# Optimization experiments

Measured on AMD Instinct MI355X. Metric: run time of the kernel, lower is better.

Reference implementation:

```python
import jax, jax.numpy as jnp
import numpy as np

N, D, H, E = 50000, 128, 512, 500000

def setup_inputs() -> dict:
    key = jax.random.key(0)
    k1, k2, k3, k4 = jax.random.split(key, 4)
    z = jax.random.normal(k1, (N, D), dtype=jnp.float32)
    edge_index = jax.random.randint(k2, (2, E), 0, N, dtype=jnp.int64)
    # torch Linear weights: fc1 [H, 2D], fc2 [1, H]
    W1 = jax.random.normal(k3, (H, 2 * D), dtype=jnp.float32) * (1.0 / np.sqrt(2 * D))
    b1 = jnp.zeros((H,), dtype=jnp.float32)
    W2 = jax.random.normal(k4, (1, H), dtype=jnp.float32) * (1.0 / np.sqrt(H))
    b2 = jnp.zeros((1,), dtype=jnp.float32)
    return {"z": z, "edge_index": edge_index, "W1": W1, "b1": b1, "W2": W2, "b2": b2}

def reference(z, edge_index, W1, b1, W2, b2):
    # gather endpoints and concat along feature dim: [E, 2D]
    z_cat = jnp.concatenate([z[edge_index[0]], z[edge_index[1]]], axis=1)
    # dropout is identity at eval (drop_rate effectively 0 for the baseline)
    h = jax.nn.relu(jnp.einsum('ef,hf->eh', z_cat, W1) + b1)  # [E, H]
    y = (jnp.einsum('eh,oh->eo', h, W2) + b2).reshape(-1)     # [E]
    return y
```

## Files before the change

kernel.cpp:

```cpp
#include <hip/hip_runtime.h>


typedef __bf16 bf16x8 __attribute__((ext_vector_type(8)));
typedef float f32x4 __attribute__((ext_vector_type(4)));

__device__ __forceinline__ unsigned short f2b(float f) {
    unsigned int u = __float_as_uint(f);
    u = (u + 0x7fffu + ((u >> 16) & 1u)) >> 16;
    return (unsigned short)u;
}

__device__ __forceinline__ void gload_lds16(const unsigned short* g, unsigned short* l) {
    __builtin_amdgcn_global_load_lds(
        (const __attribute__((address_space(1))) unsigned int*)g,
        (__attribute__((address_space(3))) unsigned int*)l, 16, 0, 0);
}

__global__ void prep_kernel(const float* __restrict__ z, const float* __restrict__ W1,
                            unsigned short* __restrict__ zb, unsigned short* __restrict__ w1s,
                            int nz4) {
    int stride = gridDim.x * blockDim.x;
    const int nw = 256 * 64;
    const int total = nz4 + nw;
    for (int idx = blockIdx.x * blockDim.x + threadIdx.x; idx < total; idx += stride) {
        if (idx < nz4) {
            float4 v = ((const float4*)z)[idx];
            ushort4 o;
            o.x = f2b(v.x); o.y = f2b(v.y); o.z = f2b(v.z); o.w = f2b(v.w);
            ((ushort4*)zb)[idx] = o;
        } else {
            int u = idx - nz4;
            int lane = u & 63;
            int blk  = u >> 6;
            int h  = (blk >> 3) * 16 + (lane & 15);
            int kb = (blk & 7) * 32 + (lane >> 4) * 8;
            const float* src = W1 + h * 256 + kb;
            ushort4 o0, o1;
            float4 v0 = *(const float4*)(src);
            float4 v1 = *(const float4*)(src + 4);
            o0.x = f2b(v0.x); o0.y = f2b(v0.y); o0.z = f2b(v0.z); o0.w = f2b(v0.w);
            o1.x = f2b(v1.x); o1.y = f2b(v1.y); o1.z = f2b(v1.z); o1.w = f2b(v1.w);
            ushort4* dst = (ushort4*)(w1s + u * 8);
            dst[0] = o0; dst[1] = o1;
        }
    }
}

__global__ __launch_bounds__(512, 2)
void edge_mlp_kernel(const int* __restrict__ ei, const unsigned short* __restrict__ zb,
                     const unsigned short* __restrict__ w1s,
                     const float* __restrict__ b1, const float* __restrict__ W2,
                     const float* __restrict__ b2p, float* __restrict__ out,
                     int E, int ntiles) {
    __shared__ unsigned short ldsA[2][64 * 256];
    __shared__ float ldsY[512];
    __shared__ float ldsB1[512];

    const int tid  = threadIdx.x;
    const int lane = tid & 63;
    const int w    = tid >> 6;
    const int l15  = lane & 15;
    const int l4   = lane >> 4;
    const int G    = gridDim.x;

    const int t0 = blockIdx.x;
    if (t0 >= ntiles) return;

    ldsB1[tid] = b1[tid];

    uint4 breg[4][8];
    #pragma unroll
    for (int j = 0; j < 4; ++j)
        #pragma unroll
        for (int kc = 0; kc < 8; ++kc)
            breg[j][kc] = *(const uint4*)(w1s + (((w * 4 + j) * 8 + kc) << 9) + lane * 8);

    f32x4 w2v[4];
    #pragma unroll
    for (int j = 0; j < 4; ++j)
        w2v[j] = *(const f32x4*)&W2[w * 64 + j * 16 + l4 * 4];
    const float b2v = b2p[0];

    const int side = (lane >> 4) & 1;
    const int rsub = lane >> 5;
    const int swz  = l15 & 7;

    asm volatile("s_waitcnt vmcnt(0)" ::: "memory");

    int ival[4];
    #pragma unroll
    for (int it = 0; it < 4; ++it) {
        int e = t0 * 64 + w * 8 + it * 2 + rsub;
        e = (e < E) ? e : (E - 1);
        ival[it] = ei[side * E + e];
    }
    #pragma unroll
    for (int it = 0; it < 4; ++it) {
        int s15 = l15 ^ ((it * 2 + rsub) & 7);
        gload_lds16(zb + (ival[it] << 7) + (s15 << 3),
                    &ldsA[0][(w * 8 + it * 2) << 8]);
    }
    asm volatile("" ::: "memory");
    {
        int t1 = t0 + G;
        #pragma unroll
        for (int it = 0; it < 4; ++it) {
            int e = t1 * 64 + w * 8 + it * 2 + rsub;
            e = (e < E) ? e : (E - 1);
            ival[it] = ei[side * E + e];
        }
    }

    int cur = 0;
    for (int t = t0; t < ntiles; t += G) {
        asm volatile("s_waitcnt vmcnt(4)" ::: "memory");
        __builtin_amdgcn_s_barrier();
        asm volatile("" ::: "memory");

        const unsigned short* bufc = &ldsA[cur][0];
        unsigned short* bufn = &ldsA[cur ^ 1][0];

        f32x4 acc[4][4];
        {
            f32x4 b1t[4];
            #pragma unroll
            for (int j = 0; j < 4; ++j)
                b1t[j] = *(const f32x4*)&ldsB1[w * 64 + j * 16 + l4 * 4];
            #pragma unroll
            for (int i = 0; i < 4; i++)
                #pragma unroll
                for (int j = 0; j < 4; j++) acc[i][j] = b1t[j];
        }

        __builtin_amdgcn_s_setprio(1);
        #pragma unroll
        for (int kc = 0; kc < 4; ++kc) {
            bf16x8 a[4];
            #pragma unroll
            for (int i = 0; i < 4; ++i)
                a[i] = *(const bf16x8*)&bufc[((l15 + 16 * i) << 8) + ((((kc << 2) + l4) ^ swz) << 3)];
            #pragma unroll
            for (int i = 0; i < 4; ++i)
                #pragma unroll
                for (int j = 0; j < 4; ++j)
                    acc[i][j] = __builtin_amdgcn_mfma_f32_16x16x32_bf16(
                        *(const bf16x8*)&breg[j][kc], a[i], acc[i][j], 0, 0, 0);
        }
        __builtin_amdgcn_s_setprio(0);

        #pragma unroll
        for (int it = 0; it < 4; ++it) {
            int s15 = l15 ^ ((it * 2 + rsub) & 7);
            gload_lds16(zb + (ival[it] << 7) + (s15 << 3),
                        bufn + ((w * 8 + it * 2) << 8));
        }
        asm volatile("" ::: "memory");

        __builtin_amdgcn_s_setprio(1);
        #pragma unroll
        for (int kc = 4; kc < 8; ++kc) {
            bf16x8 a[4];
            #pragma unroll
            for (int i = 0; i < 4; ++i)
                a[i] = *(const bf16x8*)&bufc[((l15 + 16 * i) << 8) + ((((kc << 2) + l4) ^ swz) << 3)];
            #pragma unroll
            for (int i = 0; i < 4; ++i)
                #pragma unroll
                for (int j = 0; j < 4; ++j)
                    acc[i][j] = __builtin_amdgcn_mfma_f32_16x16x32_bf16(
                        *(const bf16x8*)&breg[j][kc], a[i], acc[i][j], 0, 0, 0);
        }
        __builtin_amdgcn_s_setprio(0);

        {
            int tt = t + 2 * G;
            #pragma unroll
            for (int it = 0; it < 4; ++it) {
                int e = tt * 64 + w * 8 + it * 2 + rsub;
                e = (e < E) ? e : (E - 1);
                ival[it] = ei[side * E + e];
            }
        }

        #pragma unroll
        for (int i = 0; i < 4; i++) {
            float s = 0.f;
            #pragma unroll
            for (int j = 0; j < 4; j++)
                #pragma unroll
                for (int r = 0; r < 4; r++)
                    s = fmaf(fmaxf(acc[i][j][r], 0.f), w2v[j][r], s);
            s += __shfl_xor(s, 16);
            s += __shfl_xor(s, 32);
            if (l4 == 0) ldsY[w * 64 + i * 16 + l15] = s;
        }
        asm volatile("s_waitcnt lgkmcnt(0)" ::: "memory");
        __builtin_amdgcn_s_barrier();
        asm volatile("" ::: "memory");
        if (tid < 64) {
            int e = t * 64 + tid;
            if (e < E) {
                float v = b2v;
                #pragma unroll
                for (int k = 0; k < 8; ++k) v += ldsY[k * 64 + tid];
                out[e] = v;
            }
        }

        cur ^= 1;
    }
}

extern "C" void kernel_launch(void* const* d_in, const int* in_sizes, int n_in,
                              void* d_out, int out_size, void* d_ws, size_t ws_size,
                              hipStream_t stream) {
    const float* z  = (const float*)d_in[0];
    const int*   ei = (const int*)d_in[1];
    const float* W1 = (const float*)d_in[2];
    const float* b1 = (const float*)d_in[3];
    const float* W2 = (const float*)d_in[4];
    const float* b2 = (const float*)d_in[5];
    float* out = (float*)d_out;

    const int E  = in_sizes[1] / 2;
    const int NZ = in_sizes[0];

    unsigned short* zb  = (unsigned short*)d_ws;
    unsigned short* w1s = zb + NZ;

    prep_kernel<<<2048, 256, 0, stream>>>(z, W1, zb, w1s, NZ / 4);

    const int ntiles = (E + 63) / 64;
    int grid = ntiles < 512 ? ntiles : 512;
    edge_mlp_kernel<<<grid, 512, 0, stream>>>(ei, zb, w1s, b1, W2, b2, out, E, ntiles);
}
```

Before: 212.8 us.

## Triple-buffer gathered rows, preload edge indices into LDS, defer output reduction

Each block now preloads the edge indices for all of its tiles into LDS once at the start, instead of loading indices from global memory every iteration. The z-row gathers use three LDS buffers with a prefetch distance of two tiles, and the K loop is no longer split around the gather issue. The per-tile output reduction is deferred to the next iteration using a double-buffered ldsY and spread across all waves, which removes one barrier per tile. The index preload assumes at most 16 tiles per block, which holds for this grid and edge count. The extra buffer and index array use more LDS per block.

```diff
diff --git a/kernel.cpp b/kernel.cpp
--- a/kernel.cpp
+++ b/kernel.cpp
@@ -52,8 +52,9 @@
                      const float* __restrict__ b1, const float* __restrict__ W2,
                      const float* __restrict__ b2p, float* __restrict__ out,
                      int E, int ntiles) {
-    __shared__ unsigned short ldsA[2][64 * 256];
-    __shared__ float ldsY[512];
+    __shared__ unsigned short ldsA[3][64 * 256];
+    __shared__ int   ldsIdx[16 * 128];
+    __shared__ float ldsY[2][512];
     __shared__ float ldsB1[512];
 
     const int tid  = threadIdx.x;
@@ -62,10 +63,22 @@
     const int l15  = lane & 15;
     const int l4   = lane >> 4;
     const int G    = gridDim.x;
-
-    const int t0 = blockIdx.x;
+    const int t0   = blockIdx.x;
     if (t0 >= ntiles) return;
 
+    {
+        const int itq = tid >> 7;
+        const int sd  = (tid >> 6) & 1;
+        const int m   = tid & 63;
+        #pragma unroll
+        for (int p = 0; p < 4; ++p) {
+            int itt = p * 4 + itq;
+            int t = t0 + itt * G;
+            int e = t * 64 + m;
+            if (t >= ntiles || e >= E) e = E - 1;
+            ldsIdx[itt * 128 + sd * 64 + m] = ei[sd * E + e];
+        }
+    }
     ldsB1[tid] = b1[tid];
 
     uint4 breg[4][8];
@@ -83,42 +96,51 @@
 
     const int side = (lane >> 4) & 1;
     const int rsub = lane >> 5;
-    const int swz  = l15 & 7;
-
-    asm volatile("s_waitcnt vmcnt(0)" ::: "memory");
-
-    int ival[4];
-    #pragma unroll
-    for (int it = 0; it < 4; ++it) {
-        int e = t0 * 64 + w * 8 + it * 2 + rsub;
-        e = (e < E) ? e : (E - 1);
-        ival[it] = ei[side * E + e];
-    }
-    #pragma unroll
-    for (int it = 0; it < 4; ++it) {
-        int s15 = l15 ^ ((it * 2 + rsub) & 7);
-        gload_lds16(zb + (ival[it] << 7) + (s15 << 3),
-                    &ldsA[0][(w * 8 + it * 2) << 8]);
-    }
+
+    asm volatile("s_waitcnt vmcnt(0) lgkmcnt(0)" ::: "memory");
+    __builtin_amdgcn_s_barrier();
     asm volatile("" ::: "memory");
-    {
-        int t1 = t0 + G;
-        #pragma unroll
-        for (int it = 0; it < 4; ++it) {
-            int e = t1 * 64 + w * 8 + it * 2 + rsub;
-            e = (e < E) ? e : (E - 1);
-            ival[it] = ei[side * E + e];
-        }
-    }
-
-    int cur = 0;
-    for (int t = t0; t < ntiles; t += G) {
+
+#define ISSUE_GATHER(ITIDX, BUF)                                              \
+    do {                                                                      \
+        _Pragma("unroll")                                                     \
+        for (int q_ = 0; q_ < 4; ++q_) {                                      \
+            int m_   = w * 8 + q_ * 2 + rsub;                                 \
+            int row_ = ldsIdx[(ITIDX) * 128 + side * 64 + m_];                \
+            int s15_ = l15 ^ (m_ & 7);                                        \
+            gload_lds16(zb + (row_ << 7) + (s15_ << 3),                       \
+                        &ldsA[BUF][(w * 8 + q_ * 2) << 8]);                   \
+        }                                                                     \
+    } while (0)
+
+    ISSUE_GATHER(0, 0);
+    ISSUE_GATHER(1, 1);
+
+    int tprev = 0, pprev = 0, it = 0;
+    for (int t = t0; t < ntiles; t += G, ++it) {
+        const int p = it & 1;
         asm volatile("s_waitcnt vmcnt(4)" ::: "memory");
+        asm volatile("s_waitcnt lgkmcnt(0)" ::: "memory");
         __builtin_amdgcn_s_barrier();
         asm volatile("" ::: "memory");
 
-        const unsigned short* bufc = &ldsA[cur][0];
-        unsigned short* bufn = &ldsA[cur ^ 1][0];
+        if (it > 0 && lane < 8) {
+            int e = tprev * 64 + w * 8 + lane;
+            if (e < E) {
+                float v = b2v;
+                #pragma unroll
+                for (int k = 0; k < 8; ++k) v += ldsY[pprev][k * 64 + w * 8 + lane];
+                out[e] = v;
+            }
+        }
+
+        {
+            int itg = it + 2; if (itg > 15) itg = 15;
+            ISSUE_GATHER(itg, (it + 2) % 3);
+        }
+        asm volatile("" ::: "memory");
+
+        const unsigned short* bufc = &ldsA[it % 3][0];
 
         f32x4 acc[4][4];
         {
@@ -132,9 +154,10 @@
                 for (int j = 0; j < 4; j++) acc[i][j] = b1t[j];
         }
 
+        const int swz = l15 & 7;
         __builtin_amdgcn_s_setprio(1);
         #pragma unroll
-        for (int kc = 0; kc < 4; ++kc) {
+        for (int kc = 0; kc < 8; ++kc) {
             bf16x8 a[4];
             #pragma unroll
             for (int i = 0; i < 4; ++i)
@@ -147,40 +170,6 @@
                         *(const bf16x8*)&breg[j][kc], a[i], acc[i][j], 0, 0, 0);
         }
         __builtin_amdgcn_s_setprio(0);
-
-        #pragma unroll
-        for (int it = 0; it < 4; ++it) {
-            int s15 = l15 ^ ((it * 2 + rsub) & 7);
-            gload_lds16(zb + (ival[it] << 7) + (s15 << 3),
-                        bufn + ((w * 8 + it * 2) << 8));
-        }
-        asm volatile("" ::: "memory");
-
-        __builtin_amdgcn_s_setprio(1);
-        #pragma unroll
-        for (int kc = 4; kc < 8; ++kc) {
-            bf16x8 a[4];
-            #pragma unroll
-            for (int i = 0; i < 4; ++i)
-                a[i] = *(const bf16x8*)&bufc[((l15 + 16 * i) << 8) + ((((kc << 2) + l4) ^ swz) << 3)];
-            #pragma unroll
-            for (int i = 0; i < 4; ++i)
-                #pragma unroll
-                for (int j = 0; j < 4; ++j)
-                    acc[i][j] = __builtin_amdgcn_mfma_f32_16x16x32_bf16(
-                        *(const bf16x8*)&breg[j][kc], a[i], acc[i][j], 0, 0, 0);
-        }
-        __builtin_amdgcn_s_setprio(0);
-
-        {
-            int tt = t + 2 * G;
-            #pragma unroll
-            for (int it = 0; it < 4; ++it) {
-                int e = tt * 64 + w * 8 + it * 2 + rsub;
-                e = (e < E) ? e : (E - 1);
-                ival[it] = ei[side * E + e];
-            }
-        }
 
         #pragma unroll
         for (int i = 0; i < 4; i++) {
@@ -192,23 +181,25 @@
                     s = fmaf(fmaxf(acc[i][j][r], 0.f), w2v[j][r], s);
             s += __shfl_xor(s, 16);
             s += __shfl_xor(s, 32);
-            if (l4 == 0) ldsY[w * 64 + i * 16 + l15] = s;
-        }
-        asm volatile("s_waitcnt lgkmcnt(0)" ::: "memory");
-        __builtin_amdgcn_s_barrier();
-        asm volatile("" ::: "memory");
-        if (tid < 64) {
-            int e = t * 64 + tid;
-            if (e < E) {
-                float v = b2v;
-                #pragma unroll
-                for (int k = 0; k < 8; ++k) v += ldsY[k * 64 + tid];
-                out[e] = v;
-            }
-        }
-
-        cur ^= 1;
-    }
+            if (l4 == 0) ldsY[p][w * 64 + i * 16 + l15] = s;
+        }
+
+        tprev = t; pprev = p;
+    }
+
+    asm volatile("s_waitcnt lgkmcnt(0)" ::: "memory");
+    __builtin_amdgcn_s_barrier();
+    asm volatile("" ::: "memory");
+    if (lane < 8) {
+        int e = tprev * 64 + w * 8 + lane;
+        if (e < E) {
+            float v = b2v;
+            #pragma unroll
+            for (int k = 0; k < 8; ++k) v += ldsY[pprev][k * 64 + w * 8 + lane];
+            out[e] = v;
+        }
+    }
+#undef ISSUE_GATHER
 }
 
 extern "C" void kernel_launch(void* const* d_in, const int* in_sizes, int n_in,
```

Measured after the change: 226.2 us. 6.3% more time.

## Split hidden dim across 16 waves per 1024-thread block, halving per-wave weight registers

Applied to the files above, without the earlier changes.

Each block now runs 1024 threads (16 waves), and each wave owns 32 hidden units instead of 64. That halves the W1 fragments held in registers and the accumulator tiles per wave. W2 moves into LDS, and the final reduction sums 16 partials instead of 8. The grid is fixed at 256 persistent blocks. The aim is more waves to hide gather latency, at the cost of more barrier participants and a wider cross-wave reduction per tile. The launch_bounds(1024,4) hint may not be achievable given the roughly 70KB of LDS per block.

```diff
diff --git a/kernel.cpp b/kernel.cpp
--- a/kernel.cpp
+++ b/kernel.cpp
@@ -46,15 +46,16 @@
     }
 }
 
-__global__ __launch_bounds__(512, 2)
+__global__ __launch_bounds__(1024, 4)
 void edge_mlp_kernel(const int* __restrict__ ei, const unsigned short* __restrict__ zb,
                      const unsigned short* __restrict__ w1s,
                      const float* __restrict__ b1, const float* __restrict__ W2,
                      const float* __restrict__ b2p, float* __restrict__ out,
                      int E, int ntiles) {
     __shared__ unsigned short ldsA[2][64 * 256];
-    __shared__ float ldsY[512];
+    __shared__ float ldsY[16 * 64];
     __shared__ float ldsB1[512];
+    __shared__ float ldsW2[512];
 
     const int tid  = threadIdx.x;
     const int lane = tid & 63;
@@ -62,74 +63,78 @@
     const int l15  = lane & 15;
     const int l4   = lane >> 4;
     const int G    = gridDim.x;
-
-    const int t0 = blockIdx.x;
+    const int t0   = blockIdx.x;
     if (t0 >= ntiles) return;
 
-    ldsB1[tid] = b1[tid];
-
-    uint4 breg[4][8];
+    if (tid < 512) {
+        ldsB1[tid] = b1[tid];
+        ldsW2[tid] = W2[tid];
+    }
+
+    uint4 breg[2][8];
     #pragma unroll
-    for (int j = 0; j < 4; ++j)
+    for (int j = 0; j < 2; ++j)
         #pragma unroll
         for (int kc = 0; kc < 8; ++kc)
-            breg[j][kc] = *(const uint4*)(w1s + (((w * 4 + j) * 8 + kc) << 9) + lane * 8);
-
-    f32x4 w2v[4];
-    #pragma unroll
-    for (int j = 0; j < 4; ++j)
-        w2v[j] = *(const f32x4*)&W2[w * 64 + j * 16 + l4 * 4];
+            breg[j][kc] = *(const uint4*)(w1s + (((w * 2 + j) * 8 + kc) << 9) + lane * 8);
+
     const float b2v = b2p[0];
 
     const int side = (lane >> 4) & 1;
     const int rsub = lane >> 5;
     const int swz  = l15 & 7;
 
-    asm volatile("s_waitcnt vmcnt(0)" ::: "memory");
-
-    int ival[4];
+#define ISSUE_GATHER(BUF)                                                     \
+    do {                                                                      \
+        _Pragma("unroll")                                                     \
+        for (int q_ = 0; q_ < 2; ++q_) {                                      \
+            int m_   = w * 4 + q_ * 2 + rsub;                                 \
+            int s15_ = l15 ^ (m_ & 7);                                        \
+            gload_lds16(zb + (((long)ival[q_]) << 7) + (s15_ << 3),           \
+                        &ldsA[BUF][(w * 4 + q_ * 2) << 8]);                   \
+        }                                                                     \
+    } while (0)
+
+    asm volatile("s_waitcnt lgkmcnt(0)" ::: "memory");
+
+    int ival[2];
     #pragma unroll
-    for (int it = 0; it < 4; ++it) {
-        int e = t0 * 64 + w * 8 + it * 2 + rsub;
+    for (int q = 0; q < 2; ++q) {
+        int e = t0 * 64 + w * 4 + q * 2 + rsub;
         e = (e < E) ? e : (E - 1);
-        ival[it] = ei[side * E + e];
-    }
-    #pragma unroll
-    for (int it = 0; it < 4; ++it) {
-        int s15 = l15 ^ ((it * 2 + rsub) & 7);
-        gload_lds16(zb + (ival[it] << 7) + (s15 << 3),
-                    &ldsA[0][(w * 8 + it * 2) << 8]);
-    }
+        ival[q] = ei[side * E + e];
+    }
+    ISSUE_GATHER(0);
     asm volatile("" ::: "memory");
     {
         int t1 = t0 + G;
         #pragma unroll
-        for (int it = 0; it < 4; ++it) {
-            int e = t1 * 64 + w * 8 + it * 2 + rsub;
+        for (int q = 0; q < 2; ++q) {
+            int e = t1 * 64 + w * 4 + q * 2 + rsub;
             e = (e < E) ? e : (E - 1);
-            ival[it] = ei[side * E + e];
+            ival[q] = ei[side * E + e];
         }
     }
 
     int cur = 0;
     for (int t = t0; t < ntiles; t += G) {
-        asm volatile("s_waitcnt vmcnt(4)" ::: "memory");
+        asm volatile("s_waitcnt vmcnt(2)" ::: "memory");
         __builtin_amdgcn_s_barrier();
         asm volatile("" ::: "memory");
 
         const unsigned short* bufc = &ldsA[cur][0];
         unsigned short* bufn = &ldsA[cur ^ 1][0];
 
-        f32x4 acc[4][4];
+        f32x4 acc[4][2];
         {
-            f32x4 b1t[4];
-            #pragma unroll
-            for (int j = 0; j < 4; ++j)
-                b1t[j] = *(const f32x4*)&ldsB1[w * 64 + j * 16 + l4 * 4];
+            f32x4 b1t[2];
+            #pragma unroll
+            for (int j = 0; j < 2; ++j)
+                b1t[j] = *(const f32x4*)&ldsB1[(w * 2 + j) * 16 + l4 * 4];
             #pragma unroll
             for (int i = 0; i < 4; i++)
                 #pragma unroll
-                for (int j = 0; j < 4; j++) acc[i][j] = b1t[j];
+                for (int j = 0; j < 2; j++) acc[i][j] = b1t[j];
         }
 
         __builtin_amdgcn_s_setprio(1);
@@ -142,18 +147,13 @@
             #pragma unroll
             for (int i = 0; i < 4; ++i)
                 #pragma unroll
-                for (int j = 0; j < 4; ++j)
+                for (int j = 0; j < 2; ++j)
                     acc[i][j] = __builtin_amdgcn_mfma_f32_16x16x32_bf16(
                         *(const bf16x8*)&breg[j][kc], a[i], acc[i][j], 0, 0, 0);
         }
         __builtin_amdgcn_s_setprio(0);
 
-        #pragma unroll
-        for (int it = 0; it < 4; ++it) {
-            int s15 = l15 ^ ((it * 2 + rsub) & 7);
-            gload_lds16(zb + (ival[it] << 7) + (s15 << 3),
-                        bufn + ((w * 8 + it * 2) << 8));
-        }
+        ISSUE_GATHER(cur ^ 1);
         asm volatile("" ::: "memory");
 
         __builtin_amdgcn_s_setprio(1);
@@ -166,7 +166,7 @@
             #pragma unroll
             for (int i = 0; i < 4; ++i)
                 #pragma unroll
-                for (int j = 0; j < 4; ++j)
+                for (int j = 0; j < 2; ++j)
                     acc[i][j] = __builtin_amdgcn_mfma_f32_16x16x32_bf16(
                         *(const bf16x8*)&breg[j][kc], a[i], acc[i][j], 0, 0, 0);
         }
@@ -175,24 +175,30 @@
         {
             int tt = t + 2 * G;
             #pragma unroll
-            for (int it = 0; it < 4; ++it) {
-                int e = tt * 64 + w * 8 + it * 2 + rsub;
+            for (int q = 0; q < 2; ++q) {
+                int e = tt * 64 + w * 4 + q * 2 + rsub;
                 e = (e < E) ? e : (E - 1);
-                ival[it] = ei[side * E + e];
+                ival[q] = ei[side * E + e];
             }
         }
 
-        #pragma unroll
-        for (int i = 0; i < 4; i++) {
-            float s = 0.f;
-            #pragma unroll
-            for (int j = 0; j < 4; j++)
-                #pragma unroll
-                for (int r = 0; r < 4; r++)
-                    s = fmaf(fmaxf(acc[i][j][r], 0.f), w2v[j][r], s);
-            s += __shfl_xor(s, 16);
-            s += __shfl_xor(s, 32);
-            if (l4 == 0) ldsY[w * 64 + i * 16 + l15] = s;
+        {
+            f32x4 w2t[2];
+            #pragma unroll
+            for (int j = 0; j < 2; ++j)
+                w2t[j] = *(const f32x4*)&ldsW2[(w * 2 + j) * 16 + l4 * 4];
+            #pragma unroll
+            for (int i = 0; i < 4; i++) {
+                float s = 0.f;
+                #pragma unroll
+                for (int j = 0; j < 2; j++)
+                    #pragma unroll
+                    for (int r = 0; r < 4; r++)
+                        s = fmaf(fmaxf(acc[i][j][r], 0.f), w2t[j][r], s);
+                s += __shfl_xor(s, 16);
+                s += __shfl_xor(s, 32);
+                if (l4 == 0) ldsY[w * 64 + i * 16 + l15] = s;
+            }
         }
         asm volatile("s_waitcnt lgkmcnt(0)" ::: "memory");
         __builtin_amdgcn_s_barrier();
@@ -202,13 +208,14 @@
             if (e < E) {
                 float v = b2v;
                 #pragma unroll
-                for (int k = 0; k < 8; ++k) v += ldsY[k * 64 + tid];
+                for (int k = 0; k < 16; ++k) v += ldsY[k * 64 + tid];
                 out[e] = v;
             }
         }
 
         cur ^= 1;
     }
+#undef ISSUE_GATHER
 }
 
 extern "C" void kernel_launch(void* const* d_in, const int* in_sizes, int n_in,
@@ -231,6 +238,6 @@
     prep_kernel<<<2048, 256, 0, stream>>>(z, W1, zb, w1s, NZ / 4);
 
     const int ntiles = (E + 63) / 64;
-    int grid = ntiles < 512 ? ntiles : 512;
-    edge_mlp_kernel<<<grid, 512, 0, stream>>>(ei, zb, w1s, b1, W2, b2, out, E, ntiles);
-}
+    int grid = 256;
+    edge_mlp_kernel<<<grid, 1024, 0, stream>>>(ei, zb, w1s, b1, W2, b2, out, E, ntiles);
+}
```

After: 228.8 us. +7.5%, slower.

## Replace per-tile LDS reduction and barrier with global atomic accumulation

Applied to the files above, without the earlier changes.

Each wave now atomically adds its partial fc2 dot products straight into the output, instead of writing them to LDS, waiting at a second block barrier and summing in one wave. The output is pre-filled with b2 in the prep kernel. A dummy atomic warms the output lines, the vmcnt wait changes to 8, and the grid is fixed at 256 blocks. This removes one barrier per tile but adds eight atomics per output element and makes the float summation order nondeterministic.

```diff
diff --git a/kernel.cpp b/kernel.cpp
--- a/kernel.cpp
+++ b/kernel.cpp
@@ -17,18 +17,20 @@
 }
 
 __global__ void prep_kernel(const float* __restrict__ z, const float* __restrict__ W1,
+                            const float* __restrict__ b2p,
                             unsigned short* __restrict__ zb, unsigned short* __restrict__ w1s,
-                            int nz4) {
+                            float* __restrict__ outz, int nz4, int nout4) {
     int stride = gridDim.x * blockDim.x;
     const int nw = 256 * 64;
-    const int total = nz4 + nw;
+    const int total = nz4 + nw + nout4;
+    const float b2v = b2p[0];
     for (int idx = blockIdx.x * blockDim.x + threadIdx.x; idx < total; idx += stride) {
         if (idx < nz4) {
             float4 v = ((const float4*)z)[idx];
             ushort4 o;
             o.x = f2b(v.x); o.y = f2b(v.y); o.z = f2b(v.z); o.w = f2b(v.w);
             ((ushort4*)zb)[idx] = o;
-        } else {
+        } else if (idx < nz4 + nw) {
             int u = idx - nz4;
             int lane = u & 63;
             int blk  = u >> 6;
@@ -42,6 +44,8 @@
             o1.x = f2b(v1.x); o1.y = f2b(v1.y); o1.z = f2b(v1.z); o1.w = f2b(v1.w);
             ushort4* dst = (ushort4*)(w1s + u * 8);
             dst[0] = o0; dst[1] = o1;
+        } else {
+            ((float4*)outz)[idx - nz4 - nw] = (float4){b2v, b2v, b2v, b2v};
         }
     }
 }
@@ -50,10 +54,8 @@
 void edge_mlp_kernel(const int* __restrict__ ei, const unsigned short* __restrict__ zb,
                      const unsigned short* __restrict__ w1s,
                      const float* __restrict__ b1, const float* __restrict__ W2,
-                     const float* __restrict__ b2p, float* __restrict__ out,
-                     int E, int ntiles) {
+                     float* __restrict__ out, int E, int ntiles) {
     __shared__ unsigned short ldsA[2][64 * 256];
-    __shared__ float ldsY[512];
     __shared__ float ldsB1[512];
 
     const int tid  = threadIdx.x;
@@ -62,8 +64,7 @@
     const int l15  = lane & 15;
     const int l4   = lane >> 4;
     const int G    = gridDim.x;
-
-    const int t0 = blockIdx.x;
+    const int t0   = blockIdx.x;
     if (t0 >= ntiles) return;
 
     ldsB1[tid] = b1[tid];
@@ -79,46 +80,56 @@
     #pragma unroll
     for (int j = 0; j < 4; ++j)
         w2v[j] = *(const f32x4*)&W2[w * 64 + j * 16 + l4 * 4];
-    const float b2v = b2p[0];
 
     const int side = (lane >> 4) & 1;
     const int rsub = lane >> 5;
     const int swz  = l15 & 7;
 
-    asm volatile("s_waitcnt vmcnt(0)" ::: "memory");
+#define ISSUE_GATHER(BUF)                                                     \
+    do {                                                                      \
+        _Pragma("unroll")                                                     \
+        for (int q_ = 0; q_ < 4; ++q_) {                                      \
+            int m_   = w * 8 + q_ * 2 + rsub;                                 \
+            int s15_ = l15 ^ (m_ & 7);                                        \
+            gload_lds16(zb + (((long)ival[q_]) << 7) + (s15_ << 3),           \
+                        &ldsA[BUF][(w * 8 + q_ * 2) << 8]);                   \
+        }                                                                     \
+    } while (0)
+
+    asm volatile("s_waitcnt vmcnt(0) lgkmcnt(0)" ::: "memory");
 
     int ival[4];
     #pragma unroll
-    for (int it = 0; it < 4; ++it) {
-        int e = t0 * 64 + w * 8 + it * 2 + rsub;
+    for (int q = 0; q < 4; ++q) {
+        int e = t0 * 64 + w * 8 + q * 2 + rsub;
         e = (e < E) ? e : (E - 1);
-        ival[it] = ei[side * E + e];
-    }
-    #pragma unroll
-    for (int it = 0; it < 4; ++it) {
-        int s15 = l15 ^ ((it * 2 + rsub) & 7);
-        gload_lds16(zb + (ival[it] << 7) + (s15 << 3),
-                    &ldsA[0][(w * 8 + it * 2) << 8]);
-    }
+        ival[q] = ei[side * E + e];
+    }
+    ISSUE_GATHER(0);
     asm volatile("" ::: "memory");
     {
         int t1 = t0 + G;
         #pragma unroll
-        for (int it = 0; it < 4; ++it) {
-            int e = t1 * 64 + w * 8 + it * 2 + rsub;
+        for (int q = 0; q < 4; ++q) {
+            int e = t1 * 64 + w * 8 + q * 2 + rsub;
             e = (e < E) ? e : (E - 1);
-            ival[it] = ei[side * E + e];
-        }
+            ival[q] = ei[side * E + e];
+        }
+    }
+    asm volatile("" ::: "memory");
+    if (l4 == 0) {
+        #pragma unroll
+        for (int i = 0; i < 4; ++i)
+            atomicAdd(&out[t0 * 64 + i * 16 + l15], 0.0f);
     }
 
     int cur = 0;
     for (int t = t0; t < ntiles; t += G) {
-        asm volatile("s_waitcnt vmcnt(4)" ::: "memory");
+        asm volatile("s_waitcnt vmcnt(8)" ::: "memory");
         __builtin_amdgcn_s_barrier();
         asm volatile("" ::: "memory");
 
         const unsigned short* bufc = &ldsA[cur][0];
-        unsigned short* bufn = &ldsA[cur ^ 1][0];
 
         f32x4 acc[4][4];
         {
@@ -148,12 +159,7 @@
         }
         __builtin_amdgcn_s_setprio(0);
 
-        #pragma unroll
-        for (int it = 0; it < 4; ++it) {
-            int s15 = l15 ^ ((it * 2 + rsub) & 7);
-            gload_lds16(zb + (ival[it] << 7) + (s15 << 3),
-                        bufn + ((w * 8 + it * 2) << 8));
-        }
+        ISSUE_GATHER(cur ^ 1);
         asm volatile("" ::: "memory");
 
         __builtin_amdgcn_s_setprio(1);
@@ -175,13 +181,15 @@
         {
             int tt = t + 2 * G;
             #pragma unroll
-            for (int it = 0; it < 4; ++it) {
-                int e = tt * 64 + w * 8 + it * 2 + rsub;
+            for (int q = 0; q < 4; ++q) {
+                int e = tt * 64 + w * 8 + q * 2 + rsub;
                 e = (e < E) ? e : (E - 1);
-                ival[it] = ei[side * E + e];
+                ival[q] = ei[side * E + e];
             }
         }
-
+        asm volatile("" ::: "memory");
+
+        float s4[4];
         #pragma unroll
         for (int i = 0; i < 4; i++) {
             float s = 0.f;
@@ -192,23 +200,17 @@
                     s = fmaf(fmaxf(acc[i][j][r], 0.f), w2v[j][r], s);
             s += __shfl_xor(s, 16);
             s += __shfl_xor(s, 32);
-            if (l4 == 0) ldsY[w * 64 + i * 16 + l15] = s;
-        }
-        asm volatile("s_waitcnt lgkmcnt(0)" ::: "memory");
-        __builtin_amdgcn_s_barrier();
-        asm volatile("" ::: "memory");
-        if (tid < 64) {
-            int e = t * 64 + tid;
-            if (e < E) {
-                float v = b2v;
-                #pragma unroll
-                for (int k = 0; k < 8; ++k) v += ldsY[k * 64 + tid];
-                out[e] = v;
-            }
+            s4[i] = s;
+        }
+        #pragma unroll
+        for (int i = 0; i < 4; i++) {
+            int e = t * 64 + i * 16 + l15;
+            if (l4 == 0 && e < E) atomicAdd(&out[e], s4[i]);
         }
 
         cur ^= 1;
     }
+#undef ISSUE_GATHER
 }
 
 extern "C" void kernel_launch(void* const* d_in, const int* in_sizes, int n_in,
@@ -228,9 +230,9 @@
     unsigned short* zb  = (unsigned short*)d_ws;
     unsigned short* w1s = zb + NZ;
 
-    prep_kernel<<<2048, 256, 0, stream>>>(z, W1, zb, w1s, NZ / 4);
+    prep_kernel<<<2048, 256, 0, stream>>>(z, W1, b2, zb, w1s, out, NZ / 4, E / 4);
 
     const int ntiles = (E + 63) / 64;
-    int grid = ntiles < 512 ? ntiles : 512;
-    edge_mlp_kernel<<<grid, 512, 0, stream>>>(ei, zb, w1s, b1, W2, b2, out, E, ntiles);
-}
+    int grid = 256;
+    edge_mlp_kernel<<<grid, 512, 0, stream>>>(ei, zb, w1s, b1, W2, out, E, ntiles);
+}
```

Measured after the change: 182.8 us. 14.1% less time.
